# Optimization experiments

Measured on AMD Instinct MI355X. Metric: run time of the kernel, lower is better.

## Reference

```python
import jax, jax.numpy as jnp
import numpy as np

S, B, TD = 1024, 2, 138
D, H, Dh, L, F = 1024, 16, 64, 8, 2048
EPS = 1e-5


def setup_inputs() -> dict:
    key = jax.random.key(0)
    ks = jax.random.split(key, 32)
    std = 0.02

    def w(k, shape):
        return (jax.random.normal(k, shape, jnp.float32) * std)

    return {
        'tokens': jax.random.normal(ks[0], (S, B, TD), jnp.float32),
        'Win': w(ks[1], (D, TD)), 'bin_': jnp.zeros((D,), jnp.float32),
        'pos_emb': w(ks[2], (S, D)),
        'Wq': w(ks[3], (L, D, D)), 'bq': jnp.zeros((L, D), jnp.float32),
        'Wk': w(ks[4], (L, D, D)), 'bk': jnp.zeros((L, D), jnp.float32),
        'Wv': w(ks[5], (L, D, D)), 'bv': jnp.zeros((L, D), jnp.float32),
        'Wo': w(ks[6], (L, D, D)), 'bo': jnp.zeros((L, D), jnp.float32),
        'W1': w(ks[7], (L, F, D)), 'b1': jnp.zeros((L, F), jnp.float32),
        'W2': w(ks[8], (L, D, F)), 'b2': jnp.zeros((L, D), jnp.float32),
        'g1': jnp.ones((L, D), jnp.float32), 'be1': jnp.zeros((L, D), jnp.float32),
        'g2': jnp.ones((L, D), jnp.float32), 'be2': jnp.zeros((L, D), jnp.float32),
        'Wh': w(ks[9], (1, D)), 'bh': jnp.zeros((1,), jnp.float32),
    }


def _ln(x, g, b):
    mu = jnp.mean(x, axis=-1, keepdims=True)
    var = jnp.mean(jnp.square(x - mu), axis=-1, keepdims=True)
    return (x - mu) * jax.lax.rsqrt(var + EPS) * g + b


def _rope_tables(seq_len):
    inv_freq = 1.0 / (10000.0 ** (jnp.arange(0, Dh, 2, dtype=jnp.float32) / Dh))
    ang = jnp.arange(seq_len, dtype=jnp.float32)[:, None] * inv_freq  # (S, Dh/2)
    cos = jnp.repeat(jnp.cos(ang), 2, axis=-1)  # (S, Dh) interleaved
    sin = jnp.repeat(jnp.sin(ang), 2, axis=-1)
    return cos, sin


def _apply_rope(x, cos, sin):
    # x: (B, H, S, Dh); rotate_every_two: pairs (x0, x1) -> (-x1, x0)
    rot = jnp.stack([-x[..., 1::2], x[..., 0::2]], axis=-1).reshape(x.shape)
    return x * cos + rot * sin


def reference(tokens, Win, bin_, pos_emb, Wq, bq, Wk, bk, Wv, bv, Wo, bo,
              W1, b1, W2, b2, g1, be1, g2, be2, Wh, bh):
    s = tokens.shape[0]
    x = jnp.einsum('sbt,dt->sbd', tokens, Win) + bin_ + pos_emb[:s, None, :]
    cos, sin = _rope_tables(s)
    causal = jnp.tril(jnp.ones((s, s), dtype=bool))
    scale = 1.0 / np.sqrt(Dh)

    def to_heads(y):  # (S,B,D) -> (B,H,S,Dh)
        return jnp.transpose(y.reshape(s, -1, H, Dh), (1, 2, 0, 3))

    def layer(x, p):
        wq, bq_, wk, bk_, wv, bv_, wo, bo_, w1, b1_, w2, b2_, g1_, be1_, g2_, be2_ = p
        qh = _apply_rope(to_heads(jnp.einsum('sbd,ed->sbe', x, wq) + bq_), cos, sin)
        kh = _apply_rope(to_heads(jnp.einsum('sbd,ed->sbe', x, wk) + bk_), cos, sin)
        vh = to_heads(jnp.einsum('sbd,ed->sbe', x, wv) + bv_)
        scores = jnp.einsum('bhqd,bhkd->bhqk', qh, kh) * scale
        scores = jnp.where(causal, scores, -jnp.inf)
        attn = jax.nn.softmax(scores, axis=-1)
        o = jnp.einsum('bhqk,bhkd->bhqd', attn, vh)  # (B,H,S,Dh)
        o = jnp.transpose(o, (2, 0, 1, 3)).reshape(s, -1, D)
        attn_out = jnp.einsum('sbd,ed->sbe', o, wo) + bo_
        src2 = _ln(x + attn_out, g1_, be1_)
        ff = jnp.einsum('sbf,df->sbd', jax.nn.relu(jnp.einsum('sbd,fd->sbf', src2, w1) + b1_), w2) + b2_
        return _ln(src2 + ff, g2_, be2_), None

    params = (Wq, bq, Wk, bk, Wv, bv, Wo, bo, W1, b1, W2, b2, g1, be1, g2, be2)
    x, _ = jax.lax.scan(layer, x, params)
    return jnp.einsum('sbd,od->sbo', x, Wh) + bh  # (S, B, 1)
```

## Files before the change

### kernel.cpp

```cpp
#include <hip/hip_runtime.h>
#include <hip/hip_bf16.h>

typedef __hip_bfloat16 bf16;
typedef float f32x4 __attribute__((ext_vector_type(4)));
typedef short s16x8 __attribute__((ext_vector_type(8)));
typedef int i32x4 __attribute__((ext_vector_type(4)));

#define S_LEN 1024
#define BATCH 2
#define TDIM 138
#define KPAD 160
#define DMOD 1024
#define NHEAD 16
#define DHEAD 64
#define NLAYER 8
#define FDIM 2048
#define MROWS 2048
static const size_t DD_ = (size_t)DMOD * DMOD;
static const size_t FD_ = (size_t)FDIM * DMOD;

__device__ __forceinline__ void load_lds16(const bf16* g, bf16* l) {
  __builtin_amdgcn_global_load_lds((const __attribute__((address_space(1))) void*)g,
                                   (__attribute__((address_space(3))) void*)l, 16, 0, 0);
}

__device__ __forceinline__ unsigned pack2(float a, float b) {
  unsigned x = __builtin_bit_cast(unsigned short, __float2bfloat16(a));
  unsigned y = __builtin_bit_cast(unsigned short, __float2bfloat16(b));
  return x | (y << 16);
}

__global__ __launch_bounds__(256) void f2b_layer(
    const float4* __restrict__ Wq, const float4* __restrict__ Wk,
    const float4* __restrict__ Wv, const float4* __restrict__ Wo,
    const float4* __restrict__ W1, const float4* __restrict__ W2,
    ushort4* __restrict__ dst) {
  int i = blockIdx.x * 256 + threadIdx.x;
  const int DD4 = (int)(DD_ / 4), FD4 = (int)(FD_ / 4);
  if (i >= 4 * DD4 + 2 * FD4) return;
  const float4* src; int off;
  if (i < 3 * DD4) { int w = i / DD4; off = i - w * DD4; src = w == 0 ? Wq : (w == 1 ? Wk : Wv); }
  else if (i < 4 * DD4) { src = Wo; off = i - 3 * DD4; }
  else if (i < 4 * DD4 + FD4) { src = W1; off = i - 4 * DD4; }
  else { src = W2; off = i - 4 * DD4 - FD4; }
  float4 v = src[off];
  ushort4 o;
  o.x = __builtin_bit_cast(unsigned short, __float2bfloat16(v.x));
  o.y = __builtin_bit_cast(unsigned short, __float2bfloat16(v.y));
  o.z = __builtin_bit_cast(unsigned short, __float2bfloat16(v.z));
  o.w = __builtin_bit_cast(unsigned short, __float2bfloat16(v.w));
  dst[i] = o;
}

__global__ __launch_bounds__(256) void pad_cvt(const float* __restrict__ in,
                                               bf16* __restrict__ out, int R) {
  int i = blockIdx.x * 256 + threadIdx.x;
  if (i >= R * KPAD) return;
  int r = i / KPAD, t = i - r * KPAD;
  out[i] = __float2bfloat16(t < TDIM ? in[r * TDIM + t] : 0.0f);
}

__global__ __launch_bounds__(256) void rope_table(float2* __restrict__ t) {
  int idx = blockIdx.x * 256 + threadIdx.x;
  if (idx >= S_LEN * 32) return;
  int s = idx >> 5, i = idx & 31;
  float freq = __expf(-(float)i * (2.0f / (float)DHEAD) * 9.210340371976184f);
  float sn, cs;
  sincosf((float)s * freq, &sn, &cs);
  t[idx] = make_float2(cs, sn);
}

template<int TN, int EPI>
__global__ __launch_bounds__(256) void gemm128(
    const bf16* __restrict__ A, const bf16* __restrict__ W,
    const float* __restrict__ b0p, const float* __restrict__ b1p, const float* __restrict__ b2p,
    const float2* __restrict__ rope2, float* __restrict__ Cf,
    bf16* __restrict__ Cb0, bf16* __restrict__ Cb1, bf16* __restrict__ Cb2,
    int N, int K, int nbx) {
  constexpr int NJ = TN / 32;
  __shared__ bf16 As[128 * 32];
  __shared__ bf16 Bs[TN * 32];
  int nwg = gridDim.x, bid = blockIdx.x;
  int wg = (bid & 7) * (nwg >> 3) + (bid >> 3);
  int bx = wg % nbx, by = wg / nbx;
  int bn = bx * TN, bm = by * 128;
  int tid = threadIdx.x, lane = tid & 63, w = tid >> 6;
  int lo = lane & 15, hi = lane >> 4;
  int wr = (w >> 1) * 64, wc = (w & 1) * (TN / 2);
  f32x4 acc[4][NJ] = {};

  int srow = tid >> 2, sseg = tid & 3;
  const bf16* gA = A + (size_t)(bm + srow) * K + sseg * 8;
  const bf16* gB = W + (size_t)(bn + srow) * K + sseg * 8;
  bf16* lA = As + srow * 32 + sseg * 8;
  bf16* lB = Bs + srow * 32 + sseg * 8;

  for (int k0 = 0; k0 < K; k0 += 32) {
    load_lds16(gA + k0, lA);
    load_lds16(gA + (size_t)64 * K + k0, lA + 64 * 32);
    load_lds16(gB + k0, lB);
    if constexpr (TN == 128) load_lds16(gB + (size_t)64 * K + k0, lB + 64 * 32);
    __syncthreads();
    s16x8 af[4], bfr[NJ];
#pragma unroll
    for (int mi = 0; mi < 4; mi++) af[mi] = *(const s16x8*)(As + (wr + mi * 16 + lo) * 32 + hi * 8);
#pragma unroll
    for (int nj = 0; nj < NJ; nj++) bfr[nj] = *(const s16x8*)(Bs + (wc + nj * 16 + lo) * 32 + hi * 8);
#pragma unroll
    for (int mi = 0; mi < 4; mi++)
#pragma unroll
      for (int nj = 0; nj < NJ; nj++)
        acc[mi][nj] = __builtin_amdgcn_mfma_f32_16x16x32_bf16(af[mi], bfr[nj], acc[mi][nj], 0, 0, 0);
    __syncthreads();
  }

#pragma unroll
  for (int mi = 0; mi < 4; mi++)
#pragma unroll
    for (int nj = 0; nj < NJ; nj++)
#pragma unroll
      for (int r = 0; r < 4; r++) {
        int m = bm + wr + mi * 16 + hi * 4 + r;
        int n = bn + wc + nj * 16 + lo;
        float v = acc[mi][nj][r];
        if constexpr (EPI == 0) {
          int which = n >> 10;
          int d = n & 1023, h = d >> 6, dh = d & 63;
          int s = m >> 1, bb = m & 1;
          const float* bp = which == 0 ? b0p : (which == 1 ? b1p : b2p);
          v += bp[d];
          if (which < 2) {
            float pv = __shfl_xor(v, 1);
            float2 cn = rope2[s * 32 + (dh >> 1)];
            float o = (dh & 1) ? (v * cn.x + pv * cn.y) : (v * cn.x - pv * cn.y);
            bf16* dst = which == 0 ? Cb0 : Cb1;
            dst[(((size_t)(bb * NHEAD + h)) * S_LEN + s) * DHEAD + dh] = __float2bfloat16(o);
          } else {
            Cb2[(((size_t)(bb * NHEAD + h)) * DHEAD + dh) * S_LEN + s] = __float2bfloat16(v);
          }
        } else if constexpr (EPI == 1) {
          Cf[(size_t)m * N + n] = v + b0p[n];
        } else if constexpr (EPI == 2) {
          Cb0[(size_t)m * N + n] = __float2bfloat16(fmaxf(v + b0p[n], 0.0f));
        } else {
          float v2 = v + b0p[n] + b1p[(size_t)(m >> 1) * DMOD + n];
          Cf[(size_t)m * N + n] = v2;
          Cb0[(size_t)m * N + n] = __float2bfloat16(v2);
        }
      }
}

__global__ __launch_bounds__(256) void flash_part(const bf16* __restrict__ Q,
    const bf16* __restrict__ K, const bf16* __restrict__ Vt,
    float* __restrict__ pO, float* __restrict__ pML) {
  int bh = blockIdx.y;
  int w = threadIdx.x >> 6, lane = threadIdx.x & 63;
  int lo = lane & 15, hi = lane >> 4;
  int widx = blockIdx.x * 4 + w;
  int ch, qt;
  if (widx < 64)       { ch = 0; qt = widx; }
  else if (widx < 112) { ch = 1; qt = 16 + widx - 64; }
  else if (widx < 144) { ch = 2; qt = 32 + widx - 112; }
  else                 { ch = 3; qt = 48 + widx - 144; }
  int q0 = qt * 16, qa = q0 + lo;
  int kc0 = ch * 256;
  int kend = min(kc0 + 256, q0 + 16);
  int nkt = (kend - kc0 + 31) >> 5;

  const size_t qkb = (size_t)bh * S_LEN * DHEAD;
  const bf16* qp = Q + qkb + (size_t)qa * DHEAD + hi * 8;
  s16x8 bq0 = *(const s16x8*)qp;
  s16x8 bq1 = *(const s16x8*)(qp + 32);
  const bf16* kB = K + qkb;
  const bf16* vB = Vt + qkb;
  f32x4 accO[4] = {};
  float mv = -INFINITY, lv = 0.0f;
  const float SC = 0.18033688011112042f;

  auto loadTile = [&](int kc, s16x8& k0, s16x8& k1, s16x8& k2, s16x8& k3,
                      s16x8& v0, s16x8& v1, s16x8& v2, s16x8& v3) {
    const bf16* kp = kB + (size_t)(kc + lo) * DHEAD + hi * 8;
    k0 = *(const s16x8*)kp;
    k1 = *(const s16x8*)(kp + 32);
    k2 = *(const s16x8*)(kp + 16 * DHEAD);
    k3 = *(const s16x8*)(kp + 16 * DHEAD + 32);
    const bf16* vp = vB + (size_t)lo * S_LEN + kc + hi * 8;
    v0 = *(const s16x8*)vp;
    v1 = *(const s16x8*)(vp + (size_t)16 * S_LEN);
    v2 = *(const s16x8*)(vp + (size_t)32 * S_LEN);
    v3 = *(const s16x8*)(vp + (size_t)48 * S_LEN);
  };

  auto compute = [&](int kc, s16x8 k0, s16x8 k1, s16x8 k2, s16x8 k3,
                     s16x8 v0, s16x8 v1, s16x8 v2, s16x8 v3) {
    f32x4 st0 = {}, st1 = {};
    st0 = __builtin_amdgcn_mfma_f32_16x16x32_bf16(k0, bq0, st0, 0, 0, 0);
    st0 = __builtin_amdgcn_mfma_f32_16x16x32_bf16(k1, bq1, st0, 0, 0, 0);
    st1 = __builtin_amdgcn_mfma_f32_16x16x32_bf16(k2, bq0, st1, 0, 0, 0);
    st1 = __builtin_amdgcn_mfma_f32_16x16x32_bf16(k3, bq1, st1, 0, 0, 0);
    float p[8], pmax = -INFINITY;
    if (kc + 31 > q0) {
#pragma unroll
      for (int r = 0; r < 4; r++) {
        int k0a = kc + hi * 4 + r;
        float s0 = (k0a <= qa) ? st0[r] * SC : -INFINITY;
        float s1 = (k0a + 16 <= qa) ? st1[r] * SC : -INFINITY;
        p[r] = s0; p[4 + r] = s1;
        pmax = fmaxf(pmax, fmaxf(s0, s1));
      }
    } else {
#pragma unroll
      for (int r = 0; r < 4; r++) {
        float s0 = st0[r] * SC, s1 = st1[r] * SC;
        p[r] = s0; p[4 + r] = s1;
        pmax = fmaxf(pmax, fmaxf(s0, s1));
      }
    }
    pmax = fmaxf(pmax, __shfl_xor(pmax, 16));
    pmax = fmaxf(pmax, __shfl_xor(pmax, 32));
    float mnew = fmaxf(mv, pmax);
    float fs = exp2f(mv - mnew);
    float sum = 0.0f;
#pragma unroll
    for (int j = 0; j < 8; j++) { p[j] = exp2f(p[j] - mnew); sum += p[j]; }
    sum += __shfl_xor(sum, 16);
    sum += __shfl_xor(sum, 32);
    lv = lv * fs + sum;
    mv = mnew;
#pragma unroll
    for (int c = 0; c < 4; c++) accO[c] *= fs;
    unsigned u0 = pack2(p[0], p[1]), u1 = pack2(p[2], p[3]);
    unsigned u2 = pack2(p[4], p[5]), u3 = pack2(p[6], p[7]);
    int s1l = lo + ((hi & 1) << 5);
    int s2l = s1l + 16;
    unsigned a0 = (unsigned)__shfl((int)u0, s1l), a1 = (unsigned)__shfl((int)u1, s1l);
    unsigned a2 = (unsigned)__shfl((int)u0, s2l), a3 = (unsigned)__shfl((int)u1, s2l);
    unsigned c0 = (unsigned)__shfl((int)u2, s1l), c1 = (unsigned)__shfl((int)u3, s1l);
    unsigned c2 = (unsigned)__shfl((int)u2, s2l), c3 = (unsigned)__shfl((int)u3, s2l);
    bool lk = hi < 2;
    i32x4 pi;
    pi.x = (int)(lk ? a0 : c0); pi.y = (int)(lk ? a1 : c1);
    pi.z = (int)(lk ? a2 : c2); pi.w = (int)(lk ? a3 : c3);
    s16x8 pf = __builtin_bit_cast(s16x8, pi);
    accO[0] = __builtin_amdgcn_mfma_f32_16x16x32_bf16(v0, pf, accO[0], 0, 0, 0);
    accO[1] = __builtin_amdgcn_mfma_f32_16x16x32_bf16(v1, pf, accO[1], 0, 0, 0);
    accO[2] = __builtin_amdgcn_mfma_f32_16x16x32_bf16(v2, pf, accO[2], 0, 0, 0);
    accO[3] = __builtin_amdgcn_mfma_f32_16x16x32_bf16(v3, pf, accO[3], 0, 0, 0);
  };

  s16x8 A0, A1, A2, A3, A4, A5, A6, A7;
  s16x8 B0, B1, B2, B3, B4, B5, B6, B7;
  loadTile(kc0, A0, A1, A2, A3, A4, A5, A6, A7);
  for (int kt = 0; kt < nkt; kt += 2) {
    if (kt + 1 < nkt) loadTile(kc0 + (kt + 1) * 32, B0, B1, B2, B3, B4, B5, B6, B7);
    compute(kc0 + kt * 32, A0, A1, A2, A3, A4, A5, A6, A7);
    if (kt + 1 < nkt) {
      if (kt + 2 < nkt) loadTile(kc0 + (kt + 2) * 32, A0, A1, A2, A3, A4, A5, A6, A7);
      compute(kc0 + (kt + 1) * 32, B0, B1, B2, B3, B4, B5, B6, B7);
    }
  }

  int pbase = (bh * 64 + qt) * 4 + ch;
  float* po = pO + (size_t)pbase * 1024 + lo * 64 + hi * 4;
#pragma unroll
  for (int c = 0; c < 4; c++) *(f32x4*)(po + c * 16) = accO[c];
  if (hi == 0) {
    pML[pbase * 32 + lo] = mv;
    pML[pbase * 32 + 16 + lo] = lv;
  }
}

__global__ __launch_bounds__(256) void flash_merge(const float* __restrict__ pO,
    const float* __restrict__ pML, bf16* __restrict__ O) {
  int qt = blockIdx.x, bh = blockIdx.y;
  int b = bh >> 4, h = bh & 15;
  int nch = (qt >> 4) + 1;
  int t = threadIdx.x;
  int dh = t & 63, r0 = t >> 6;
  int pb0 = (bh * 64 + qt) * 4;
#pragma unroll
  for (int j = 0; j < 4; j++) {
    int row = r0 + j * 4;
    float ms = -INFINITY;
    for (int i = 0; i < nch; i++) ms = fmaxf(ms, pML[(pb0 + i) * 32 + row]);
    float l = 0.0f, o = 0.0f;
    for (int i = 0; i < nch; i++) {
      float wgt = exp2f(pML[(pb0 + i) * 32 + row] - ms);
      l += wgt * pML[(pb0 + i) * 32 + 16 + row];
      o += wgt * pO[(size_t)(pb0 + i) * 1024 + row * 64 + dh];
    }
    int q = qt * 16 + row;
    O[((size_t)q * BATCH + b) * DMOD + h * DHEAD + dh] = __float2bfloat16(o / l);
  }
}

__global__ __launch_bounds__(256) void ln_kernel(const float* __restrict__ a,
    const float* __restrict__ r, const float* __restrict__ g,
    const float* __restrict__ be, float* __restrict__ outf, bf16* __restrict__ outb) {
  int m = blockIdx.x;
  int tid = threadIdx.x;
  float vals[4];
  float s1 = 0.f, s2 = 0.f;
  for (int j = 0; j < 4; j++) {
    int d = tid + j * 256;
    float v = a[(size_t)m * DMOD + d] + r[(size_t)m * DMOD + d];
    vals[j] = v; s1 += v; s2 += v * v;
  }
  __shared__ float red[8];
  for (int d = 1; d < 64; d <<= 1) { s1 += __shfl_xor(s1, d); s2 += __shfl_xor(s2, d); }
  int w = tid >> 6, lane = tid & 63;
  if (lane == 0) { red[w] = s1; red[4 + w] = s2; }
  __syncthreads();
  s1 = red[0] + red[1] + red[2] + red[3];
  s2 = red[4] + red[5] + red[6] + red[7];
  float mean = s1 * (1.0f / DMOD);
  float var = s2 * (1.0f / DMOD) - mean * mean;
  float rstd = rsqrtf(var + 1e-5f);
  for (int j = 0; j < 4; j++) {
    int d = tid + j * 256;
    float o = (vals[j] - mean) * rstd * g[d] + be[d];
    outf[(size_t)m * DMOD + d] = o;
    outb[(size_t)m * DMOD + d] = __float2bfloat16(o);
  }
}

__global__ __launch_bounds__(256) void head_kernel(const float* __restrict__ x,
    const float* __restrict__ Wh, const float* __restrict__ bh, float* __restrict__ out) {
  int m = blockIdx.x * 4 + (threadIdx.x >> 6);
  int lane = threadIdx.x & 63;
  float s = 0.f;
  for (int j = 0; j < 16; j++) {
    int d = lane + j * 64;
    s += x[(size_t)m * DMOD + d] * Wh[d];
  }
  for (int d = 1; d < 64; d <<= 1) s += __shfl_xor(s, d);
  if (lane == 0) out[m] = s + bh[0];
}

extern "C" void kernel_launch(void* const* d_in, const int* in_sizes, int n_in,
                              void* d_out, int out_size, void* d_ws, size_t ws_size,
                              hipStream_t stream) {
  (void)in_sizes; (void)n_in; (void)out_size; (void)ws_size;
  const float* tokens = (const float*)d_in[0];
  const float* Win    = (const float*)d_in[1];
  const float* binp   = (const float*)d_in[2];
  const float* pos    = (const float*)d_in[3];
  const float* Wq     = (const float*)d_in[4];
  const float* bq     = (const float*)d_in[5];
  const float* Wk     = (const float*)d_in[6];
  const float* bk     = (const float*)d_in[7];
  const float* Wv     = (const float*)d_in[8];
  const float* bv     = (const float*)d_in[9];
  const float* Wo     = (const float*)d_in[10];
  const float* bo     = (const float*)d_in[11];
  const float* W1     = (const float*)d_in[12];
  const float* b1     = (const float*)d_in[13];
  const float* W2     = (const float*)d_in[14];
  const float* b2     = (const float*)d_in[15];
  const float* g1     = (const float*)d_in[16];
  const float* be1    = (const float*)d_in[17];
  const float* g2     = (const float*)d_in[18];
  const float* be2    = (const float*)d_in[19];
  const float* Wh     = (const float*)d_in[20];
  const float* bhp    = (const float*)d_in[21];
  float* out = (float*)d_out;

  char* p = (char*)d_ws;
  auto alloc = [&](size_t bytes) { char* r = p; p += (bytes + 255) & ~(size_t)255; return r; };
  float* xf   = (float*)alloc((size_t)MROWS * DMOD * 4);
  bf16*  xb   = (bf16*) alloc((size_t)MROWS * DMOD * 2);
  float* x2f  = (float*)alloc((size_t)MROWS * DMOD * 4);
  bf16*  x2b  = (bf16*) alloc((size_t)MROWS * DMOD * 2);
  float* tmpf = (float*)alloc((size_t)MROWS * DMOD * 4);
  bf16*  qb   = (bf16*) alloc((size_t)MROWS * DMOD * 2);
  bf16*  kb   = (bf16*) alloc((size_t)MROWS * DMOD * 2);
  bf16*  vt   = (bf16*) alloc((size_t)MROWS * DMOD * 2);
  bf16*  ob   = (bf16*) alloc((size_t)MROWS * DMOD * 2);
  bf16*  hb   = (bf16*) alloc((size_t)MROWS * FDIM * 2);
  bf16*  wb   = (bf16*) alloc((4 * DD_ + 2 * FD_) * 2);
  bf16*  tokb = (bf16*) alloc((size_t)MROWS * KPAD * 2);
  bf16*  winb = (bf16*) alloc((size_t)DMOD * KPAD * 2);
  float2* rope2 = (float2*)alloc((size_t)S_LEN * 32 * 8);
  float* pO   = (float*)alloc((size_t)32 * 64 * 4 * 1024 * 4);
  float* pML  = (float*)alloc((size_t)32 * 64 * 4 * 32 * 4);

  rope_table<<<(S_LEN * 32 + 255) / 256, 256, 0, stream>>>(rope2);
  pad_cvt<<<(MROWS * KPAD + 255) / 256, 256, 0, stream>>>(tokens, tokb, MROWS);
  pad_cvt<<<(DMOD * KPAD + 255) / 256, 256, 0, stream>>>(Win, winb, DMOD);
  gemm128<128, 3><<<128, 256, 0, stream>>>(
      tokb, winb, binp, pos, nullptr, nullptr,
      xf, xb, nullptr, nullptr, DMOD, KPAD, 8);

  const int nW4 = (int)((4 * DD_ + 2 * FD_) / 4);

  for (int l = 0; l < NLAYER; l++) {
    f2b_layer<<<(nW4 + 255) / 256, 256, 0, stream>>>(
        (const float4*)(Wq + l * DD_), (const float4*)(Wk + l * DD_),
        (const float4*)(Wv + l * DD_), (const float4*)(Wo + l * DD_),
        (const float4*)(W1 + l * FD_), (const float4*)(W2 + l * FD_), (ushort4*)wb);

    gemm128<128, 0><<<384, 256, 0, stream>>>(
        xb, wb, bq + l * DMOD, bk + l * DMOD, bv + l * DMOD, rope2,
        nullptr, qb, kb, vt, 3 * DMOD, DMOD, 24);

    flash_part<<<dim3(40, BATCH * NHEAD), 256, 0, stream>>>(qb, kb, vt, pO, pML);
    flash_merge<<<dim3(S_LEN / 16, BATCH * NHEAD), 256, 0, stream>>>(pO, pML, ob);

    gemm128<64, 1><<<256, 256, 0, stream>>>(
        ob, wb + 3 * DD_, bo + l * DMOD, nullptr, nullptr, nullptr,
        tmpf, nullptr, nullptr, nullptr, DMOD, DMOD, 16);

    ln_kernel<<<MROWS, 256, 0, stream>>>(xf, tmpf, g1 + l * DMOD, be1 + l * DMOD, x2f, x2b);

    gemm128<128, 2><<<256, 256, 0, stream>>>(
        x2b, wb + 4 * DD_, b1 + l * FDIM, nullptr, nullptr, nullptr,
        nullptr, hb, nullptr, nullptr, FDIM, DMOD, 16);

    gemm128<64, 1><<<256, 256, 0, stream>>>(
        hb, wb + 4 * DD_ + FD_, b2 + l * DMOD, nullptr, nullptr, nullptr,
        tmpf, nullptr, nullptr, nullptr, DMOD, FDIM, 16);

    ln_kernel<<<MROWS, 256, 0, stream>>>(x2f, tmpf, g2 + l * DMOD, be2 + l * DMOD, xf, xb);
  }

  head_kernel<<<MROWS / 4, 256, 0, stream>>>(xf, Wh, bhp, out);
}
```

Measured before the change: 1.640 ms.

## Rework split-K flash attention to 32x32 MFMA tiles with XCD-aware block mapping

The split-K flash attention partial kernel moves from 16-row query tiles with 16x16x32 MFMAs to 32-row query tiles with 32x32x16 MFMAs. Key chunks shrink from 256 to 128 keys, which gives 8 chunks and 144 warps per head. Blocks are flattened to a 1D grid and remapped so each XCD handles a contiguous set of heads, which aims to improve L2 locality of K/V. The merge kernel is updated to match the new partial layout, and the explicit double-buffered register prefetch of K/V tiles is removed. That removal may expose more load latency.

```diff
diff --git a/kernel.cpp b/kernel.cpp
--- a/kernel.cpp
+++ b/kernel.cpp
@@ -3,6 +3,7 @@
 
 typedef __hip_bfloat16 bf16;
 typedef float f32x4 __attribute__((ext_vector_type(4)));
+typedef float f32x16 __attribute__((ext_vector_type(16)));
 typedef short s16x8 __attribute__((ext_vector_type(8)));
 typedef int i32x4 __attribute__((ext_vector_type(4)));
 
@@ -153,143 +154,139 @@
 __global__ __launch_bounds__(256) void flash_part(const bf16* __restrict__ Q,
     const bf16* __restrict__ K, const bf16* __restrict__ Vt,
     float* __restrict__ pO, float* __restrict__ pML) {
-  int bh = blockIdx.y;
+  int bid = blockIdx.x;
+  int xcd = bid & 7, idx = bid >> 3;
+  int bh = xcd * 4 + idx / 36;
   int w = threadIdx.x >> 6, lane = threadIdx.x & 63;
-  int lo = lane & 15, hi = lane >> 4;
-  int widx = blockIdx.x * 4 + w;
-  int ch, qt;
-  if (widx < 64)       { ch = 0; qt = widx; }
-  else if (widx < 112) { ch = 1; qt = 16 + widx - 64; }
-  else if (widx < 144) { ch = 2; qt = 32 + widx - 112; }
-  else                 { ch = 3; qt = 48 + widx - 144; }
-  int q0 = qt * 16, qa = q0 + lo;
-  int kc0 = ch * 256;
-  int kend = min(kc0 + 256, q0 + 16);
+  int widx = (idx % 36) * 4 + w;
+  int c = 0;
+  while (c < 7 && widx >= (c + 1) * (32 - 2 * c)) c++;
+  int qt = widx - c * (30 - 2 * c);
+  int l31 = lane & 31, hi1 = lane >> 5;
+  int q0 = qt * 32, kc0 = c * 128;
+  int kend = min(kc0 + 128, q0 + 32);
   int nkt = (kend - kc0 + 31) >> 5;
 
   const size_t qkb = (size_t)bh * S_LEN * DHEAD;
-  const bf16* qp = Q + qkb + (size_t)qa * DHEAD + hi * 8;
-  s16x8 bq0 = *(const s16x8*)qp;
-  s16x8 bq1 = *(const s16x8*)(qp + 32);
-  const bf16* kB = K + qkb;
-  const bf16* vB = Vt + qkb;
-  f32x4 accO[4] = {};
+  const bf16* qp = Q + qkb + (size_t)(q0 + l31) * DHEAD + hi1 * 8;
+  s16x8 bq0 = *(const s16x8*)(qp);
+  s16x8 bq1 = *(const s16x8*)(qp + 16);
+  s16x8 bq2 = *(const s16x8*)(qp + 32);
+  s16x8 bq3 = *(const s16x8*)(qp + 48);
+  f32x16 accO0 = {}, accO1 = {};
   float mv = -INFINITY, lv = 0.0f;
   const float SC = 0.18033688011112042f;
 
-  auto loadTile = [&](int kc, s16x8& k0, s16x8& k1, s16x8& k2, s16x8& k3,
-                      s16x8& v0, s16x8& v1, s16x8& v2, s16x8& v3) {
-    const bf16* kp = kB + (size_t)(kc + lo) * DHEAD + hi * 8;
-    k0 = *(const s16x8*)kp;
-    k1 = *(const s16x8*)(kp + 32);
-    k2 = *(const s16x8*)(kp + 16 * DHEAD);
-    k3 = *(const s16x8*)(kp + 16 * DHEAD + 32);
-    const bf16* vp = vB + (size_t)lo * S_LEN + kc + hi * 8;
-    v0 = *(const s16x8*)vp;
-    v1 = *(const s16x8*)(vp + (size_t)16 * S_LEN);
-    v2 = *(const s16x8*)(vp + (size_t)32 * S_LEN);
-    v3 = *(const s16x8*)(vp + (size_t)48 * S_LEN);
-  };
-
-  auto compute = [&](int kc, s16x8 k0, s16x8 k1, s16x8 k2, s16x8 k3,
-                     s16x8 v0, s16x8 v1, s16x8 v2, s16x8 v3) {
-    f32x4 st0 = {}, st1 = {};
-    st0 = __builtin_amdgcn_mfma_f32_16x16x32_bf16(k0, bq0, st0, 0, 0, 0);
-    st0 = __builtin_amdgcn_mfma_f32_16x16x32_bf16(k1, bq1, st0, 0, 0, 0);
-    st1 = __builtin_amdgcn_mfma_f32_16x16x32_bf16(k2, bq0, st1, 0, 0, 0);
-    st1 = __builtin_amdgcn_mfma_f32_16x16x32_bf16(k3, bq1, st1, 0, 0, 0);
-    float p[8], pmax = -INFINITY;
-    if (kc + 31 > q0) {
-#pragma unroll
-      for (int r = 0; r < 4; r++) {
-        int k0a = kc + hi * 4 + r;
-        float s0 = (k0a <= qa) ? st0[r] * SC : -INFINITY;
-        float s1 = (k0a + 16 <= qa) ? st1[r] * SC : -INFINITY;
-        p[r] = s0; p[4 + r] = s1;
-        pmax = fmaxf(pmax, fmaxf(s0, s1));
+  for (int kt = 0; kt < nkt; kt++) {
+    int kc = kc0 + kt * 32;
+    const bf16* kp = K + qkb + (size_t)(kc + l31) * DHEAD + hi1 * 8;
+    s16x8 ka0 = *(const s16x8*)(kp);
+    s16x8 ka1 = *(const s16x8*)(kp + 16);
+    s16x8 ka2 = *(const s16x8*)(kp + 32);
+    s16x8 ka3 = *(const s16x8*)(kp + 48);
+    const bf16* vp = Vt + qkb + (size_t)l31 * S_LEN + kc + hi1 * 8;
+    s16x8 va00 = *(const s16x8*)(vp);
+    s16x8 va01 = *(const s16x8*)(vp + 16);
+    s16x8 va10 = *(const s16x8*)(vp + (size_t)32 * S_LEN);
+    s16x8 va11 = *(const s16x8*)(vp + (size_t)32 * S_LEN + 16);
+
+    f32x16 st = {};
+    st = __builtin_amdgcn_mfma_f32_32x32x16_bf16(ka0, bq0, st, 0, 0, 0);
+    st = __builtin_amdgcn_mfma_f32_32x32x16_bf16(ka1, bq1, st, 0, 0, 0);
+    st = __builtin_amdgcn_mfma_f32_32x32x16_bf16(ka2, bq2, st, 0, 0, 0);
+    st = __builtin_amdgcn_mfma_f32_32x32x16_bf16(ka3, bq3, st, 0, 0, 0);
+
+    bool diag = (kc >= q0);
+    float pmax = -INFINITY;
+#pragma unroll
+    for (int j = 0; j < 16; j++) {
+      float s = st[j] * SC;
+      if (diag) {
+        int krow = kc + (j & 3) + 8 * (j >> 2) + 4 * hi1;
+        if (krow > q0 + l31) s = -INFINITY;
       }
-    } else {
-#pragma unroll
-      for (int r = 0; r < 4; r++) {
-        float s0 = st0[r] * SC, s1 = st1[r] * SC;
-        p[r] = s0; p[4 + r] = s1;
-        pmax = fmaxf(pmax, fmaxf(s0, s1));
-      }
+      st[j] = s;
+      pmax = fmaxf(pmax, s);
     }
-    pmax = fmaxf(pmax, __shfl_xor(pmax, 16));
     pmax = fmaxf(pmax, __shfl_xor(pmax, 32));
     float mnew = fmaxf(mv, pmax);
     float fs = exp2f(mv - mnew);
     float sum = 0.0f;
 #pragma unroll
-    for (int j = 0; j < 8; j++) { p[j] = exp2f(p[j] - mnew); sum += p[j]; }
-    sum += __shfl_xor(sum, 16);
+    for (int j = 0; j < 16; j++) {
+      float e = exp2f(st[j] - mnew);
+      st[j] = e;
+      sum += e;
+    }
     sum += __shfl_xor(sum, 32);
     lv = lv * fs + sum;
     mv = mnew;
-#pragma unroll
-    for (int c = 0; c < 4; c++) accO[c] *= fs;
-    unsigned u0 = pack2(p[0], p[1]), u1 = pack2(p[2], p[3]);
-    unsigned u2 = pack2(p[4], p[5]), u3 = pack2(p[6], p[7]);
-    int s1l = lo + ((hi & 1) << 5);
-    int s2l = s1l + 16;
-    unsigned a0 = (unsigned)__shfl((int)u0, s1l), a1 = (unsigned)__shfl((int)u1, s1l);
-    unsigned a2 = (unsigned)__shfl((int)u0, s2l), a3 = (unsigned)__shfl((int)u1, s2l);
-    unsigned c0 = (unsigned)__shfl((int)u2, s1l), c1 = (unsigned)__shfl((int)u3, s1l);
-    unsigned c2 = (unsigned)__shfl((int)u2, s2l), c3 = (unsigned)__shfl((int)u3, s2l);
-    bool lk = hi < 2;
-    i32x4 pi;
-    pi.x = (int)(lk ? a0 : c0); pi.y = (int)(lk ? a1 : c1);
-    pi.z = (int)(lk ? a2 : c2); pi.w = (int)(lk ? a3 : c3);
-    s16x8 pf = __builtin_bit_cast(s16x8, pi);
-    accO[0] = __builtin_amdgcn_mfma_f32_16x16x32_bf16(v0, pf, accO[0], 0, 0, 0);
-    accO[1] = __builtin_amdgcn_mfma_f32_16x16x32_bf16(v1, pf, accO[1], 0, 0, 0);
-    accO[2] = __builtin_amdgcn_mfma_f32_16x16x32_bf16(v2, pf, accO[2], 0, 0, 0);
-    accO[3] = __builtin_amdgcn_mfma_f32_16x16x32_bf16(v3, pf, accO[3], 0, 0, 0);
-  };
-
-  s16x8 A0, A1, A2, A3, A4, A5, A6, A7;
-  s16x8 B0, B1, B2, B3, B4, B5, B6, B7;
-  loadTile(kc0, A0, A1, A2, A3, A4, A5, A6, A7);
-  for (int kt = 0; kt < nkt; kt += 2) {
-    if (kt + 1 < nkt) loadTile(kc0 + (kt + 1) * 32, B0, B1, B2, B3, B4, B5, B6, B7);
-    compute(kc0 + kt * 32, A0, A1, A2, A3, A4, A5, A6, A7);
-    if (kt + 1 < nkt) {
-      if (kt + 2 < nkt) loadTile(kc0 + (kt + 2) * 32, A0, A1, A2, A3, A4, A5, A6, A7);
-      compute(kc0 + (kt + 1) * 32, B0, B1, B2, B3, B4, B5, B6, B7);
-    }
-  }
-
-  int pbase = (bh * 64 + qt) * 4 + ch;
-  float* po = pO + (size_t)pbase * 1024 + lo * 64 + hi * 4;
-#pragma unroll
-  for (int c = 0; c < 4; c++) *(f32x4*)(po + c * 16) = accO[c];
-  if (hi == 0) {
-    pML[pbase * 32 + lo] = mv;
-    pML[pbase * 32 + 16 + lo] = lv;
+    accO0 = accO0 * fs;
+    accO1 = accO1 * fs;
+
+    unsigned w0 = pack2(st[0], st[1]),   w1 = pack2(st[2], st[3]);
+    unsigned w2 = pack2(st[4], st[5]),   w3 = pack2(st[6], st[7]);
+    unsigned w4 = pack2(st[8], st[9]),   w5 = pack2(st[10], st[11]);
+    unsigned w6 = pack2(st[12], st[13]), w7 = pack2(st[14], st[15]);
+    unsigned xw0 = (unsigned)__shfl_xor((int)w0, 32), xw1 = (unsigned)__shfl_xor((int)w1, 32);
+    unsigned xw2 = (unsigned)__shfl_xor((int)w2, 32), xw3 = (unsigned)__shfl_xor((int)w3, 32);
+    unsigned xw4 = (unsigned)__shfl_xor((int)w4, 32), xw5 = (unsigned)__shfl_xor((int)w5, 32);
+    unsigned xw6 = (unsigned)__shfl_xor((int)w6, 32), xw7 = (unsigned)__shfl_xor((int)w7, 32);
+    bool hb = (hi1 != 0);
+    i32x4 f0, f1;
+    f0.x = (int)(hb ? xw2 : w0); f0.y = (int)(hb ? xw3 : w1);
+    f0.z = (int)(hb ? w2 : xw0); f0.w = (int)(hb ? w3 : xw1);
+    f1.x = (int)(hb ? xw6 : w4); f1.y = (int)(hb ? xw7 : w5);
+    f1.z = (int)(hb ? w6 : xw4); f1.w = (int)(hb ? w7 : xw5);
+    s16x8 pf0 = __builtin_bit_cast(s16x8, f0);
+    s16x8 pf1 = __builtin_bit_cast(s16x8, f1);
+    accO0 = __builtin_amdgcn_mfma_f32_32x32x16_bf16(va00, pf0, accO0, 0, 0, 0);
+    accO0 = __builtin_amdgcn_mfma_f32_32x32x16_bf16(va01, pf1, accO0, 0, 0, 0);
+    accO1 = __builtin_amdgcn_mfma_f32_32x32x16_bf16(va10, pf0, accO1, 0, 0, 0);
+    accO1 = __builtin_amdgcn_mfma_f32_32x32x16_bf16(va11, pf1, accO1, 0, 0, 0);
+  }
+
+  int pbase = bh * 144 + widx;
+  float* po = pO + (size_t)pbase * 2048 + l31 * 64 + 4 * hi1;
+#pragma unroll
+  for (int jj = 0; jj < 4; jj++) {
+    f32x4 v0 = {accO0[4 * jj], accO0[4 * jj + 1], accO0[4 * jj + 2], accO0[4 * jj + 3]};
+    f32x4 v1 = {accO1[4 * jj], accO1[4 * jj + 1], accO1[4 * jj + 2], accO1[4 * jj + 3]};
+    *(f32x4*)(po + 8 * jj) = v0;
+    *(f32x4*)(po + 32 + 8 * jj) = v1;
+  }
+  if (hi1 == 0) {
+    pML[pbase * 64 + l31] = mv;
+    pML[pbase * 64 + 32 + l31] = lv;
   }
 }
 
 __global__ __launch_bounds__(256) void flash_merge(const float* __restrict__ pO,
     const float* __restrict__ pML, bf16* __restrict__ O) {
-  int qt = blockIdx.x, bh = blockIdx.y;
+  int bid = blockIdx.x;
+  int xcd = bid & 7, idx = bid >> 3;
+  int bh = xcd * 4 + idx / 32, qt = idx % 32;
   int b = bh >> 4, h = bh & 15;
-  int nch = (qt >> 4) + 1;
+  int nch = (qt >> 2) + 1;
   int t = threadIdx.x;
   int dh = t & 63, r0 = t >> 6;
-  int pb0 = (bh * 64 + qt) * 4;
-#pragma unroll
-  for (int j = 0; j < 4; j++) {
-    int row = r0 + j * 4;
+  int ibase = bh * 144;
+#pragma unroll
+  for (int j = 0; j < 8; j++) {
+    int row = j * 4 + r0;
     float ms = -INFINITY;
-    for (int i = 0; i < nch; i++) ms = fmaxf(ms, pML[(pb0 + i) * 32 + row]);
+    for (int cc = 0; cc < nch; cc++) {
+      int wi = cc * (30 - 2 * cc) + qt;
+      ms = fmaxf(ms, pML[(ibase + wi) * 64 + row]);
+    }
     float l = 0.0f, o = 0.0f;
-    for (int i = 0; i < nch; i++) {
-      float wgt = exp2f(pML[(pb0 + i) * 32 + row] - ms);
-      l += wgt * pML[(pb0 + i) * 32 + 16 + row];
-      o += wgt * pO[(size_t)(pb0 + i) * 1024 + row * 64 + dh];
+    for (int cc = 0; cc < nch; cc++) {
+      int wi = cc * (30 - 2 * cc) + qt;
+      float wgt = exp2f(pML[(ibase + wi) * 64 + row] - ms);
+      l += wgt * pML[(ibase + wi) * 64 + 32 + row];
+      o += wgt * pO[(size_t)(ibase + wi) * 2048 + row * 64 + dh];
     }
-    int q = qt * 16 + row;
+    int q = qt * 32 + row;
     O[((size_t)q * BATCH + b) * DMOD + h * DHEAD + dh] = __float2bfloat16(o / l);
   }
 }
@@ -381,8 +378,8 @@
   bf16*  tokb = (bf16*) alloc((size_t)MROWS * KPAD * 2);
   bf16*  winb = (bf16*) alloc((size_t)DMOD * KPAD * 2);
   float2* rope2 = (float2*)alloc((size_t)S_LEN * 32 * 8);
-  float* pO   = (float*)alloc((size_t)32 * 64 * 4 * 1024 * 4);
-  float* pML  = (float*)alloc((size_t)32 * 64 * 4 * 32 * 4);
+  float* pO   = (float*)alloc((size_t)32 * 144 * 2048 * 4);
+  float* pML  = (float*)alloc((size_t)32 * 144 * 64 * 4);
 
   rope_table<<<(S_LEN * 32 + 255) / 256, 256, 0, stream>>>(rope2);
   pad_cvt<<<(MROWS * KPAD + 255) / 256, 256, 0, stream>>>(tokens, tokb, MROWS);
@@ -403,8 +400,8 @@
         xb, wb, bq + l * DMOD, bk + l * DMOD, bv + l * DMOD, rope2,
         nullptr, qb, kb, vt, 3 * DMOD, DMOD, 24);
 
-    flash_part<<<dim3(40, BATCH * NHEAD), 256, 0, stream>>>(qb, kb, vt, pO, pML);
-    flash_merge<<<dim3(S_LEN / 16, BATCH * NHEAD), 256, 0, stream>>>(pO, pML, ob);
+    flash_part<<<1152, 256, 0, stream>>>(qb, kb, vt, pO, pML);
+    flash_merge<<<1024, 256, 0, stream>>>(pO, pML, ob);
 
     gemm128<64, 1><<<256, 256, 0, stream>>>(
         ob, wb + 3 * DD_, bo + l * DMOD, nullptr, nullptr, nullptr,
```

New measurement: 1.770 ms. +7.9%, slower.
